# Performance work log

Hardware: AMD Instinct MI355X
Metric: run time of the kernel (lower is better)

The kernel has to match this reference:

```python
import jax, jax.numpy as jnp
import numpy as np

B, T, D = 8, 1024, 128
TEMP = 0.1
WEIGHT = 1.0


def _neg_scaled_l2(x, y):
    # x: [P, T, D], y: [P, S, D] -> -||x-y||^2 / D / TEMP  (l2 similarity, normalize_dimension=True)
    x2 = jnp.sum(x * x, axis=-1)[..., :, None]            # [P, T, 1]
    y2 = jnp.sum(y * y, axis=-1)[..., None, :]            # [P, 1, S]
    xy = jnp.einsum('ptd,psd->pts', x, y)                 # [P, T, S]
    d2 = jnp.maximum(x2 + y2 - 2.0 * xy, 0.0)             # cdist(...)**2 is non-negative
    return -d2 / D / TEMP


def setup_inputs() -> dict:
    key = jax.random.key(0)
    k1, k2, k3 = jax.random.split(key, 3)
    embs = jax.random.normal(k1, (B, T, D), dtype=jnp.float32)
    frame_idxs = jnp.sort(jax.random.randint(k2, (B, T), 0, 4096, dtype=jnp.int32), axis=-1)
    video_len = jax.random.randint(k3, (B,), T, 4096, dtype=jnp.int32)
    return {"embs": embs, "frame_idxs": frame_idxs, "video_len": video_len}


def reference(embs, frame_idxs, video_len):
    # All ordered pairs (i, j) with i != j, built at trace time.
    pairs = np.array([(i, j) for i in range(B) for j in range(B) if i != j])
    ii, jj = pairs[:, 0], pairs[:, 1]                     # [P]

    e1 = embs[ii]                                         # [P, T, D]
    e2 = embs[jj]                                         # [P, T, D]

    # Cycle: soft nearest neighbors of e1 in e2, then align back to e1.
    sim12 = _neg_scaled_l2(e1, e2)                        # [P, T, T]
    beta12 = jax.nn.softmax(sim12, axis=-1)
    nn_embs = jnp.einsum('pts,psd->ptd', beta12, e2)      # [P, T, D]
    logits = _neg_scaled_l2(nn_embs, e1)                  # [P, T, T]

    beta = jax.nn.softmax(logits, axis=-1)                # [P, T, T]
    steps = frame_idxs.astype(jnp.float32) / video_len.astype(jnp.float32)[:, None]  # [B, T]
    sp = steps[ii]                                        # [P, T] (steps of sequence i)
    time_true = sp                                        # one_hot(labels) picks the diagonal
    time_pred = jnp.einsum('pts,ps->pt', beta, sp)        # [P, T]
    loss = jnp.mean((time_pred - time_true) ** 2)
    return WEIGHT * loss
```

## Files before the change

kernel.cpp:

```cpp
#include <hip/hip_runtime.h>
#include <hip/hip_bf16.h>


#define T_ 1024
#define D_ 128
#define NPAIR 56
#define NSCALE 0.11271055006945026f
#define SQDS 0.474785316f

typedef float f32x16 __attribute__((ext_vector_type(16)));
typedef unsigned short u16x8 __attribute__((ext_vector_type(8)));

#define B8F 131072
#define B8T 163840

__device__ __forceinline__ unsigned short f2bf(float f) {
  unsigned u = __float_as_uint(f);
  u += 0x7fff + ((u >> 16) & 1);
  return (unsigned short)(u >> 16);
}
__device__ __forceinline__ float bf2f(unsigned short v) {
  return __uint_as_float(((unsigned)v) << 16);
}
__device__ __forceinline__ float clamp8(float x) {
  return fminf(fmaxf(x, -440.f), 440.f);
}
__device__ __forceinline__ unsigned pk4(float a, float b, float c, float d) {
  int w = __builtin_amdgcn_cvt_pk_fp8_f32(a, b, 0, false);
  w = __builtin_amdgcn_cvt_pk_fp8_f32(c, d, w, true);
  return (unsigned)w;
}
__device__ __forceinline__ float waveSum(float v) {
#pragma unroll
  for (int k = 32; k >= 1; k >>= 1) v += __shfl_xor(v, k, 64);
  return v;
}
__device__ __forceinline__ void stage1k(const unsigned char* g, unsigned char* lds, int lane) {
  __builtin_amdgcn_global_load_lds(
      (const __attribute__((address_space(1))) unsigned int*)(g + lane * 16),
      (__attribute__((address_space(3))) unsigned int*)lds, 16, 0, 0);
}

__device__ __forceinline__ void c2b8(const unsigned* m, int lh, long long* b0, long long* b1) {
  unsigned send0 = lh ? m[0] : m[1];
  unsigned send1 = lh ? m[2] : m[3];
  unsigned r0 = (unsigned)__shfl_xor((int)send0, 32, 64);
  unsigned r1 = (unsigned)__shfl_xor((int)send1, 32, 64);
  union { unsigned u[2]; long long ll; } x0, x1;
  x0.u[0] = lh ? r0 : m[0];  x0.u[1] = lh ? m[1] : r0;
  x1.u[0] = lh ? r1 : m[2];  x1.u[1] = lh ? m[3] : r1;
  *b0 = x0.ll; *b1 = x1.ll;
}

#define MFMA8(A, B, C) __builtin_amdgcn_mfma_f32_32x32x16_fp8_fp8((A), (B), (C), 0, 0, 0)
#define LD8(P, Q) (*(const long long*)((P) + (Q) * 512))
#define EXPC(x) fminf(__builtin_amdgcn_exp2f(x), 448.f)
#define WAITV(N) asm volatile("s_waitcnt vmcnt(" #N ")" ::: "memory")
#define BAR() do { asm volatile("" ::: "memory"); __builtin_amdgcn_s_barrier(); asm volatile("" ::: "memory"); } while (0)

__global__ __launch_bounds__(256) void convert_kernel(
    const float* __restrict__ embs, const int* __restrict__ fi,
    const int* __restrict__ vl, unsigned char* __restrict__ e8F,
    unsigned char* __restrict__ e8T, float* __restrict__ steps,
    float* __restrict__ acc, unsigned* __restrict__ cnt) {
  __shared__ unsigned short tileS[32 * 136];
  __shared__ float psum[32][8];
  __shared__ float g_sh[32], sp_sh[32];
  const int b = blockIdx.x >> 5;
  const int t0 = (blockIdx.x & 31) * 32;
  const int tid = threadIdx.x;
  const int row = tid >> 3, seg = tid & 7;

  if (blockIdx.x == 0 && tid == 0) { acc[0] = 0.f; cnt[0] = 0u; }

  const float* src = embs + (size_t)(b * T_ + t0 + row) * D_ + seg * 16;
  float4 g4[4];
#pragma unroll
  for (int k = 0; k < 4; k++) g4[k] = ((const float4*)src)[k];
  float s = 0.f;
  float fv[16];
#pragma unroll
  for (int k = 0; k < 4; k++) {
    s += g4[k].x * g4[k].x + g4[k].y * g4[k].y + g4[k].z * g4[k].z + g4[k].w * g4[k].w;
    fv[4 * k + 0] = g4[k].x * SQDS; fv[4 * k + 1] = g4[k].y * SQDS;
    fv[4 * k + 2] = g4[k].z * SQDS; fv[4 * k + 3] = g4[k].w * SQDS;
  }
  psum[row][seg] = s;

  {
    unsigned char* dstA = e8F + (size_t)b * B8F + (size_t)((t0 >> 5) * 8 + seg) * 512;
    uint2 lo, hi;
    lo.x = pk4(fv[0], fv[1], fv[2], fv[3]);   lo.y = pk4(fv[4], fv[5], fv[6], fv[7]);
    hi.x = pk4(fv[8], fv[9], fv[10], fv[11]); hi.y = pk4(fv[12], fv[13], fv[14], fv[15]);
    *(uint2*)(dstA + row * 8) = lo;
    *(uint2*)(dstA + (size_t)(32 + row) * 8) = hi;
  }
#pragma unroll
  for (int k = 0; k < 16; k++) tileS[row * 136 + seg * 16 + k] = f2bf(fv[k]);
  __syncthreads();

  if (tid < 32) {
    float t = 0.f;
#pragma unroll
    for (int k = 0; k < 8; k++) t += psum[tid][k];
    int gr = b * T_ + t0 + tid;
    float sp = (float)fi[gr] / (float)vl[b];
    steps[gr] = sp;
    sp_sh[tid] = sp;
    g_sh[tid] = __builtin_amdgcn_exp2f(14.0f - t * NSCALE);
  }
  __syncthreads();

  {
    const int c8 = tid >> 5;
    const int n2 = c8 & 3, scp = c8 >> 2;
    const int dd = n2 * 32 + (tid & 31);
#pragma unroll
    for (int half = 0; half < 2; half++) {
      const int lane = half * 32 + (tid & 31);
      const int sl = scp * 16 + half * 8;
      float vv[8];
#pragma unroll
      for (int jj = 0; jj < 8; jj++)
        vv[jj] = clamp8(bf2f(tileS[(sl + jj) * 136 + dd]) * g_sh[sl + jj]);
      uint2 wv;
      wv.x = pk4(vv[0], vv[1], vv[2], vv[3]);
      wv.y = pk4(vv[4], vv[5], vv[6], vv[7]);
      int c = n2 * 64 + (t0 >> 4) + scp;
      *(uint2*)(e8T + (size_t)b * B8T + (size_t)c * 512 + lane * 8) = wv;
    }
  }
  if (tid < 128) {
    const int sc2 = tid >> 6, lane = tid & 63;
    const int m = lane & 31, kh = lane >> 5;
    uint2 wv; wv.x = 0u; wv.y = 0u;
    if (m < 2) {
      float vv[8];
#pragma unroll
      for (int e = 0; e < 8; e++) {
        int sl = sc2 * 16 + kh * 8 + e;
        float gg = g_sh[sl];
        vv[e] = clamp8(m ? gg * sp_sh[sl] : gg);
      }
      wv.x = pk4(vv[0], vv[1], vv[2], vv[3]);
      wv.y = pk4(vv[4], vv[5], vv[6], vv[7]);
    }
    int c = 256 + (t0 >> 4) + sc2;
    *(uint2*)(e8T + (size_t)b * B8T + (size_t)c * 512 + lane * 8) = wv;
  }
}

__global__ __launch_bounds__(256, 2) void tcc_main(
    const unsigned char* __restrict__ e8F, const unsigned char* __restrict__ e8T,
    const float* __restrict__ steps, float* __restrict__ loss_acc,
    unsigned* __restrict__ cnt, float* __restrict__ out) {
  __shared__ unsigned char smem[55296];
  __shared__ float blred[4];
  unsigned char* kt = smem;
  unsigned char* vt = smem + 24576;
  unsigned char* gt = smem + 24576;

  const int bx = blockIdx.x;
  const int pair = bx >> 3;
  const int tile = bx & 7;
  const int i = pair / 7;
  const int r = pair % 7;
  const int j = r + (r >= i ? 1 : 0);
  const int tid = threadIdx.x;
  const int w = tid >> 6;
  const int l = tid & 63;
  const int l31 = l & 31;
  const int lh = l >> 5;
  const int tb = tile * 128 + w * 32;

  const unsigned char* eFi = e8F + (size_t)i * B8F;
  const unsigned char* eFj = e8F + (size_t)j * B8F;
  const unsigned char* eTj = e8T + (size_t)j * B8T;
  const unsigned char* eTi = e8T + (size_t)i * B8T;

  long long qf8[8];
  {
    const unsigned char* qb = eFi + (size_t)((tb >> 5) * 8) * 512 + l * 8;
#pragma unroll
    for (int kc = 0; kc < 8; kc++) qf8[kc] = LD8(qb, kc);
  }

  const f32x16 Z = {0.f, 0.f, 0.f, 0.f, 0.f, 0.f, 0.f, 0.f,
                    0.f, 0.f, 0.f, 0.f, 0.f, 0.f, 0.f, 0.f};
  const f32x16 CM6 = {-6.f, -6.f, -6.f, -6.f, -6.f, -6.f, -6.f, -6.f,
                      -6.f, -6.f, -6.f, -6.f, -6.f, -6.f, -6.f, -6.f};
  f32x16 o[5];
#pragma unroll
  for (int n2 = 0; n2 < 5; n2++) o[n2] = Z;

  auto stageP1 = [&](int t, int b) {
    stage1k(eFj + (size_t)(8 * t + 2 * w) * 1024, kt + b * 8192 + (2 * w) * 1024, l);
    stage1k(eFj + (size_t)(8 * t + 2 * w + 1) * 1024, kt + b * 8192 + (2 * w + 1) * 1024, l);
#pragma unroll
    for (int u = 0; u < 3; u++) {
      int vu = w + 4 * u;
      if (vu < 10) {
        int n2v = vu >> 1, uh = vu & 1;
        stage1k(eTj + (size_t)(n2v * 32 + t * 2 + uh) * 1024, vt + b * 10240 + vu * 1024, l);
      }
    }
  };
  auto stageP2 = [&](int t, int b) {
    stage1k(eFi + (size_t)(8 * t + 2 * w) * 1024, kt + b * 8192 + (2 * w) * 1024, l);
    stage1k(eFi + (size_t)(8 * t + 2 * w + 1) * 1024, kt + b * 8192 + (2 * w + 1) * 1024, l);
    if (w < 2) stage1k(eTi + (size_t)(128 + t * 2 + w) * 1024, gt + b * 2048 + w * 1024, l);
  };

  stageP1(0, 0);
  stageP1(1, 1);
  if (w < 2) WAITV(5); else WAITV(4);
  BAR();

  {
    int cur = 0, pre = 2;
    for (int st = 0; st < 16; st++) {
      if (st <= 13) stageP1(st + 2, pre);
      __builtin_amdgcn_sched_barrier(0);

      const unsigned char* kb = kt + cur * 8192 + l * 8;
      const unsigned char* vb = vt + cur * 10240 + l * 8;

      f32x16 ca0 = MFMA8(LD8(kb, 0), qf8[0], CM6);
      f32x16 ca1 = MFMA8(LD8(kb, 8), qf8[0], CM6);
#pragma unroll
      for (int dc = 1; dc < 8; dc++) {
        ca0 = MFMA8(LD8(kb, dc), qf8[dc], ca0);
        ca1 = MFMA8(LD8(kb, 8 + dc), qf8[dc], ca1);
      }
      unsigned m0[4], m1[4];
#pragma unroll
      for (int k2 = 0; k2 < 4; k2++) {
        m0[k2] = pk4(EXPC(ca0[4 * k2]), EXPC(ca0[4 * k2 + 1]),
                     EXPC(ca0[4 * k2 + 2]), EXPC(ca0[4 * k2 + 3]));
        m1[k2] = pk4(EXPC(ca1[4 * k2]), EXPC(ca1[4 * k2 + 1]),
                     EXPC(ca1[4 * k2 + 2]), EXPC(ca1[4 * k2 + 3]));
      }
      long long pB[4];
      c2b8(m0, lh, &pB[0], &pB[1]);
      c2b8(m1, lh, &pB[2], &pB[3]);
#pragma unroll
      for (int n2 = 0; n2 < 5; n2++)
#pragma unroll
        for (int sc = 0; sc < 4; sc++)
          o[n2] = MFMA8(LD8(vb, n2 * 4 + sc), pB[sc], o[n2]);

      if (st <= 13) {
        if (w < 2) WAITV(5); else WAITV(4);
        BAR();
      } else if (st == 14) {
        WAITV(0);
        BAR();
      } else {
        BAR();
      }
      cur = (cur == 2) ? 0 : cur + 1;
      pre = (pre == 2) ? 0 : pre + 1;
    }
  }

  stageP2(0, 0);
  stageP2(1, 1);

  float Lme = o[4][0];
  float Lo = __shfl_xor(Lme, 32, 64);
  float inv = 1.0f / (lh ? Lo : Lme);
  long long qf2[8];
#pragma unroll
  for (int n2 = 0; n2 < 4; n2++) {
    unsigned mm[4];
#pragma unroll
    for (int k2 = 0; k2 < 4; k2++)
      mm[k2] = pk4(o[n2][4 * k2] * inv, o[n2][4 * k2 + 1] * inv,
                   o[n2][4 * k2 + 2] * inv, o[n2][4 * k2 + 3] * inv);
    c2b8(mm, lh, &qf2[2 * n2], &qf2[2 * n2 + 1]);
  }
  f32x16 acc6 = Z;
  if (w < 2) WAITV(3); else WAITV(2);
  BAR();

  {
    int cur = 0, pre = 2;
    for (int st = 0; st < 16; st++) {
      if (st <= 13) stageP2(st + 2, pre);
      __builtin_amdgcn_sched_barrier(0);

      const unsigned char* kb = kt + cur * 8192 + l * 8;
      const unsigned char* gb = gt + cur * 2048 + l * 8;

      f32x16 ca0 = MFMA8(LD8(kb, 0), qf2[0], CM6);
      f32x16 ca1 = MFMA8(LD8(kb, 8), qf2[0], CM6);
#pragma unroll
      for (int dc = 1; dc < 8; dc++) {
        ca0 = MFMA8(LD8(kb, dc), qf2[dc], ca0);
        ca1 = MFMA8(LD8(kb, 8 + dc), qf2[dc], ca1);
      }
      unsigned m0[4], m1[4];
#pragma unroll
      for (int k2 = 0; k2 < 4; k2++) {
        m0[k2] = pk4(EXPC(ca0[4 * k2]), EXPC(ca0[4 * k2 + 1]),
                     EXPC(ca0[4 * k2 + 2]), EXPC(ca0[4 * k2 + 3]));
        m1[k2] = pk4(EXPC(ca1[4 * k2]), EXPC(ca1[4 * k2 + 1]),
                     EXPC(ca1[4 * k2 + 2]), EXPC(ca1[4 * k2 + 3]));
      }
      long long pB[4];
      c2b8(m0, lh, &pB[0], &pB[1]);
      c2b8(m1, lh, &pB[2], &pB[3]);
#pragma unroll
      for (int sc = 0; sc < 4; sc++)
        acc6 = MFMA8(LD8(gb, sc), pB[sc], acc6);

      if (st <= 13) {
        if (w < 2) WAITV(3); else WAITV(2);
        BAR();
      } else if (st == 14) {
        WAITV(0);
        BAR();
      }
      cur = (cur == 2) ? 0 : cur + 1;
      pre = (pre == 2) ? 0 : pre + 1;
    }
  }

  float local = 0.f;
  if (lh == 0) {
    float pred = acc6[1] / acc6[0];
    float tt = steps[i * T_ + tb + l31];
    float dd = pred - tt;
    local = dd * dd;
  }
  local = waveSum(local);
  if (l == 0) blred[w] = local;
  __syncthreads();
  if (tid == 0) {
    atomicAdd(loss_acc, blred[0] + blred[1] + blred[2] + blred[3]);
    __threadfence();
    unsigned old = atomicAdd(cnt, 1u);
    if (old == (unsigned)(gridDim.x - 1)) {
      float v = atomicAdd(loss_acc, 0.0f);
      out[0] = v * (1.0f / (float)(NPAIR * T_));
    }
  }
}

extern "C" void kernel_launch(void* const* d_in, const int* in_sizes, int n_in,
                              void* d_out, int out_size, void* d_ws, size_t ws_size,
                              hipStream_t stream) {
  const float* embs = (const float*)d_in[0];
  const int* frame_idxs = (const int*)d_in[1];
  const int* video_len = (const int*)d_in[2];
  float* out = (float*)d_out;

  char* ws = (char*)d_ws;
  float* acc = (float*)ws;
  unsigned* cnt = (unsigned*)(ws + 512);
  float* steps = (float*)(ws + 4096);
  unsigned char* e8F = (unsigned char*)(ws + 65536);
  unsigned char* e8T = e8F + (size_t)8 * B8F;

  convert_kernel<<<dim3(256), dim3(256), 0, stream>>>(embs, frame_idxs, video_len,
                                                      e8F, e8T, steps, acc, cnt);
  tcc_main<<<dim3(NPAIR * 8), dim3(256), 0, stream>>>(e8F, e8T, steps, acc, cnt, out);
}
```

Measured before the change: 117.5 us.

## Software-pipeline QK MFMA one tile ahead of softmax and PV in both phases

```diff
diff --git a/kernel.cpp b/kernel.cpp
--- a/kernel.cpp
+++ b/kernel.cpp
@@ -9,7 +9,6 @@
 #define SQDS 0.474785316f
 
 typedef float f32x16 __attribute__((ext_vector_type(16)));
-typedef unsigned short u16x8 __attribute__((ext_vector_type(8)));
 
 #define B8F 131072
 #define B8T 163840
@@ -213,25 +212,39 @@
 
   stageP1(0, 0);
   stageP1(1, 1);
-  if (w < 2) WAITV(5); else WAITV(4);
+  WAITV(0);
   BAR();
 
-  {
-    int cur = 0, pre = 2;
+  f32x16 ca0, ca1;
+  {
+    const unsigned char* kb = kt + l * 8;
+    ca0 = MFMA8(LD8(kb, 0), qf8[0], CM6);
+    ca1 = MFMA8(LD8(kb, 8), qf8[0], CM6);
+#pragma unroll
+    for (int dc = 1; dc < 8; dc++) {
+      ca0 = MFMA8(LD8(kb, dc), qf8[dc], ca0);
+      ca1 = MFMA8(LD8(kb, 8 + dc), qf8[dc], ca1);
+    }
+  }
+
+  {
+    int cur = 0, nxt = 1, pre = 2;
     for (int st = 0; st < 16; st++) {
       if (st <= 13) stageP1(st + 2, pre);
       __builtin_amdgcn_sched_barrier(0);
 
-      const unsigned char* kb = kt + cur * 8192 + l * 8;
-      const unsigned char* vb = vt + cur * 10240 + l * 8;
-
-      f32x16 ca0 = MFMA8(LD8(kb, 0), qf8[0], CM6);
-      f32x16 ca1 = MFMA8(LD8(kb, 8), qf8[0], CM6);
-#pragma unroll
-      for (int dc = 1; dc < 8; dc++) {
-        ca0 = MFMA8(LD8(kb, dc), qf8[dc], ca0);
-        ca1 = MFMA8(LD8(kb, 8 + dc), qf8[dc], ca1);
-      }
+      f32x16 cb0, cb1;
+      if (st < 15) {
+        const unsigned char* kb = kt + nxt * 8192 + l * 8;
+        cb0 = MFMA8(LD8(kb, 0), qf8[0], CM6);
+        cb1 = MFMA8(LD8(kb, 8), qf8[0], CM6);
+#pragma unroll
+        for (int dc = 1; dc < 8; dc++) {
+          cb0 = MFMA8(LD8(kb, dc), qf8[dc], cb0);
+          cb1 = MFMA8(LD8(kb, 8 + dc), qf8[dc], cb1);
+        }
+      }
+
       unsigned m0[4], m1[4];
 #pragma unroll
       for (int k2 = 0; k2 < 4; k2++) {
@@ -243,6 +256,8 @@
       long long pB[4];
       c2b8(m0, lh, &pB[0], &pB[1]);
       c2b8(m1, lh, &pB[2], &pB[3]);
+
+      const unsigned char* vb = vt + cur * 10240 + l * 8;
 #pragma unroll
       for (int n2 = 0; n2 < 5; n2++)
 #pragma unroll
@@ -250,16 +265,13 @@
           o[n2] = MFMA8(LD8(vb, n2 * 4 + sc), pB[sc], o[n2]);
 
       if (st <= 13) {
-        if (w < 2) WAITV(5); else WAITV(4);
-        BAR();
-      } else if (st == 14) {
         WAITV(0);
         BAR();
-      } else {
+      } else if (st == 15) {
         BAR();
       }
-      cur = (cur == 2) ? 0 : cur + 1;
-      pre = (pre == 2) ? 0 : pre + 1;
+      if (st < 15) { ca0 = cb0; ca1 = cb1; }
+      int tswap = cur; cur = nxt; nxt = pre; pre = tswap;
     }
   }
 
@@ -280,49 +292,62 @@
     c2b8(mm, lh, &qf2[2 * n2], &qf2[2 * n2 + 1]);
   }
   f32x16 acc6 = Z;
-  if (w < 2) WAITV(3); else WAITV(2);
+  WAITV(0);
   BAR();
 
-  {
-    int cur = 0, pre = 2;
+  f32x16 da0, da1;
+  {
+    const unsigned char* kb = kt + l * 8;
+    da0 = MFMA8(LD8(kb, 0), qf2[0], CM6);
+    da1 = MFMA8(LD8(kb, 8), qf2[0], CM6);
+#pragma unroll
+    for (int dc = 1; dc < 8; dc++) {
+      da0 = MFMA8(LD8(kb, dc), qf2[dc], da0);
+      da1 = MFMA8(LD8(kb, 8 + dc), qf2[dc], da1);
+    }
+  }
+
+  {
+    int cur = 0, nxt = 1, pre = 2;
     for (int st = 0; st < 16; st++) {
       if (st <= 13) stageP2(st + 2, pre);
       __builtin_amdgcn_sched_barrier(0);
 
-      const unsigned char* kb = kt + cur * 8192 + l * 8;
-      const unsigned char* gb = gt + cur * 2048 + l * 8;
-
-      f32x16 ca0 = MFMA8(LD8(kb, 0), qf2[0], CM6);
-      f32x16 ca1 = MFMA8(LD8(kb, 8), qf2[0], CM6);
-#pragma unroll
-      for (int dc = 1; dc < 8; dc++) {
-        ca0 = MFMA8(LD8(kb, dc), qf2[dc], ca0);
-        ca1 = MFMA8(LD8(kb, 8 + dc), qf2[dc], ca1);
-      }
+      f32x16 db0, db1;
+      if (st < 15) {
+        const unsigned char* kb = kt + nxt * 8192 + l * 8;
+        db0 = MFMA8(LD8(kb, 0), qf2[0], CM6);
+        db1 = MFMA8(LD8(kb, 8), qf2[0], CM6);
+#pragma unroll
+        for (int dc = 1; dc < 8; dc++) {
+          db0 = MFMA8(LD8(kb, dc), qf2[dc], db0);
+          db1 = MFMA8(LD8(kb, 8 + dc), qf2[dc], db1);
+        }
+      }
+
       unsigned m0[4], m1[4];
 #pragma unroll
       for (int k2 = 0; k2 < 4; k2++) {
-        m0[k2] = pk4(EXPC(ca0[4 * k2]), EXPC(ca0[4 * k2 + 1]),
-                     EXPC(ca0[4 * k2 + 2]), EXPC(ca0[4 * k2 + 3]));
-        m1[k2] = pk4(EXPC(ca1[4 * k2]), EXPC(ca1[4 * k2 + 1]),
-                     EXPC(ca1[4 * k2 + 2]), EXPC(ca1[4 * k2 + 3]));
+        m0[k2] = pk4(EXPC(da0[4 * k2]), EXPC(da0[4 * k2 + 1]),
+                     EXPC(da0[4 * k2 + 2]), EXPC(da0[4 * k2 + 3]));
+        m1[k2] = pk4(EXPC(da1[4 * k2]), EXPC(da1[4 * k2 + 1]),
+                     EXPC(da1[4 * k2 + 2]), EXPC(da1[4 * k2 + 3]));
       }
       long long pB[4];
       c2b8(m0, lh, &pB[0], &pB[1]);
       c2b8(m1, lh, &pB[2], &pB[3]);
+
+      const unsigned char* gb = gt + cur * 2048 + l * 8;
 #pragma unroll
       for (int sc = 0; sc < 4; sc++)
         acc6 = MFMA8(LD8(gb, sc), pB[sc], acc6);
 
       if (st <= 13) {
-        if (w < 2) WAITV(3); else WAITV(2);
-        BAR();
-      } else if (st == 14) {
         WAITV(0);
         BAR();
       }
-      cur = (cur == 2) ? 0 : cur + 1;
-      pre = (pre == 2) ? 0 : pre + 1;
+      if (st < 15) { da0 = db0; da1 = db1; }
+      int tswap = cur; cur = nxt; nxt = pre; pre = tswap;
     }
   }
 
```

Result: faster. 114.4 us (-2.6%).
